# Kernel tuning notes

Measured on AMD Instinct MI355X. Metric: run time of the kernel, lower is better.

Reference implementation:

```python
import jax, jax.numpy as jnp
import numpy as np

HEADS = 16
DIM_HEAD = 64
DIM = 1024
INNER = HEADS * DIM_HEAD


def setup_inputs() -> dict:
    key = jax.random.key(0)
    k1, k2, k3, k4 = jax.random.split(key, 4)
    x = jax.random.normal(k1, (4, 2048, DIM), dtype=jnp.float32)
    W_qkv = jax.random.normal(k2, (DIM, 3 * INNER), dtype=jnp.float32) * (DIM ** -0.5)
    W_out = jax.random.normal(k3, (INNER, DIM), dtype=jnp.float32) * (INNER ** -0.5)
    b_out = jax.random.normal(k4, (DIM,), dtype=jnp.float32) * 0.01
    temperature = jnp.asarray(np.log(DIM_HEAD ** -0.5), dtype=jnp.float32)
    return {"x": x, "W_qkv": W_qkv, "W_out": W_out, "b_out": b_out,
            "temperature": temperature}


def reference(x, W_qkv, W_out, b_out, temperature):
    b, n, _ = x.shape
    qkv = jnp.einsum('bnd,de->bne', x, W_qkv)  # [b, n, 3*inner]
    q, k, v = jnp.split(qkv, 3, axis=-1)
    def split_heads(t):
        return t.reshape(b, n, HEADS, DIM_HEAD).transpose(0, 2, 1, 3)  # b h n d
    q, k, v = split_heads(q), split_heads(k), split_heads(v)
    scale = jnp.exp(temperature)
    dots = jnp.einsum('bhid,bhjd->bhij', q, k) * scale  # [b, h, n, n]
    mask_value = -jnp.finfo(dots.dtype).max
    eye = jnp.eye(n, dtype=bool)
    dots = jnp.where(eye, mask_value, dots)
    attn = jax.nn.softmax(dots, axis=-1)
    out = jnp.einsum('bhij,bhjd->bhid', attn, v)  # [b, h, n, d]
    out = out.transpose(0, 2, 1, 3).reshape(b, n, INNER)
    return jnp.einsum('bni,id->bnd', out, W_out) + b_out
```

## Files before the change

kernel.cpp:

```cpp
#include <hip/hip_runtime.h>


using u16 = unsigned short;
typedef short short8 __attribute__((ext_vector_type(8)));
typedef float floatx4 __attribute__((ext_vector_type(4)));
typedef float floatx16 __attribute__((ext_vector_type(16)));
typedef unsigned int uint2v __attribute__((ext_vector_type(2)));

#define B_ 4
#define N_ 2048
#define H_ 16
#define DH_ 64
#define D_ 1024
#define INNER_ 1024
#define M_ (B_ * N_)

__device__ __forceinline__ float bf2f(u16 h) {
    union { unsigned u; float f; } c; c.u = ((unsigned)h) << 16; return c.f;
}
__device__ __forceinline__ u16 f2bf(float f) {
    union { float f; unsigned u; } c; c.f = f;
    unsigned u = c.u + 0x7fffu + ((c.u >> 16) & 1u);
    return (u16)(u >> 16);
}
__device__ __forceinline__ unsigned cvtpk_bf16(float lo, float hi) {
    unsigned r;
    asm("v_cvt_pk_bf16_f32 %0, %1, %2" : "=v"(r) : "v"(lo), "v"(hi));
    return r;
}
__device__ __forceinline__ float fast_exp2(float x) {
#if defined(__has_builtin) && __has_builtin(__builtin_amdgcn_exp2f)
    return __builtin_amdgcn_exp2f(x);
#else
    return __expf(x * 0.69314718056f);
#endif
}
__device__ __forceinline__ void gl2lds16(const u16* g, u16* l) {
    __builtin_amdgcn_global_load_lds(
        (const __attribute__((address_space(1))) void*)g,
        (__attribute__((address_space(3))) void*)l, 16, 0, 0);
}

__global__ void detect_dtype(const u16* __restrict__ x, int* __restrict__ flag) {
    __shared__ int cnt;
    if (threadIdx.x == 0) cnt = 0;
    __syncthreads();
    int c = 0;
    for (int i = threadIdx.x; i < 4096; i += 256) {
        int e = (x[i] >> 7) & 0xFF;
        if (e >= 107 && e <= 147) c++;
    }
    atomicAdd(&cnt, c);
    __syncthreads();
    if (threadIdx.x == 0) flag[0] = (cnt >= 3584) ? 1 : 0;
}

__global__ __launch_bounds__(256) void convert_x(
    const void* __restrict__ in, u16* __restrict__ out, int n,
    const int* __restrict__ flag) {
    int f = flag[0];
    int i0 = (blockIdx.x * 256 + threadIdx.x) * 8;
    if (f) {
        const u16* p = (const u16*)in;
        for (int i = 0; i < 8; i++) out[i0 + i] = p[i0 + i];
    } else {
        const float* p = (const float*)in;
        for (int i = 0; i < 8; i++) out[i0 + i] = f2bf(p[i0 + i]);
    }
}

__global__ void prep_misc(const void* __restrict__ bias_in,
                          const void* __restrict__ temp_in,
                          float* __restrict__ bias_f, float* __restrict__ temp_f,
                          const int* __restrict__ flag) {
    int f = flag[0];
    for (int i = threadIdx.x; i < 1024; i += 256)
        bias_f[i] = f ? bf2f(((const u16*)bias_in)[i]) : ((const float*)bias_in)[i];
    if (threadIdx.x == 0)
        temp_f[0] = f ? bf2f(((const u16*)temp_in)[0]) : ((const float*)temp_in)[0];
}

__global__ __launch_bounds__(256) void transpose_cvt(
    const void* __restrict__ in, u16* __restrict__ out, int R, int C,
    const int* __restrict__ flag) {
    __shared__ u16 t[32][33];
    int f = flag[0];
    int tx = threadIdx.x & 31, ty = threadIdx.x >> 5;
    int c0 = blockIdx.x * 32, r0 = blockIdx.y * 32;
    for (int i = 0; i < 4; i++) {
        long idx = (long)(r0 + ty + i * 8) * C + c0 + tx;
        t[ty + i * 8][tx] = f ? ((const u16*)in)[idx] : f2bf(((const float*)in)[idx]);
    }
    __syncthreads();
    for (int i = 0; i < 4; i++)
        out[(long)(c0 + ty + i * 8) * R + r0 + tx] = t[tx][ty + i * 8];
}

__global__ __launch_bounds__(256) void transpose_v(
    const u16* __restrict__ in, u16* __restrict__ out) {
    __shared__ u16 t[32][33];
    const int bh = blockIdx.z;
    const u16* src = in + (long)bh * N_ * DH_;
    u16* dst = out + (long)bh * DH_ * N_;
    int tx = threadIdx.x & 31, ty = threadIdx.x >> 5;
    int r0 = blockIdx.y * 32;
    int c0 = blockIdx.x * 32;
    for (int i = 0; i < 4; i++)
        t[ty + i * 8][tx] = src[(long)(r0 + ty + i * 8) * DH_ + c0 + tx];
    __syncthreads();
    for (int i = 0; i < 4; i++)
        dst[(long)(c0 + ty + i * 8) * N_ + r0 + tx] = t[tx][ty + i * 8];
}

template <int MODE>
__global__ __launch_bounds__(256) void gemm_bt(
    const u16* __restrict__ A, const u16* __restrict__ Bt,
    int M, int N, int K,
    u16* __restrict__ out0, u16* __restrict__ out1, u16* __restrict__ out2,
    void* __restrict__ outv, const float* __restrict__ bias,
    const int* __restrict__ flag, const float* __restrict__ temp_f) {
    __shared__ __align__(16) u16 lA[128 * 32];
    __shared__ __align__(16) u16 lB[128 * 32];
    const int tid = threadIdx.x;
    const int lane = tid & 63;
    const int w = tid >> 6;
    const int wr = w >> 1, wc = w & 1;
    const int qd = lane >> 4, qm = lane & 15;
    const long m0 = (long)blockIdx.x * 128;
    const long n0 = (long)blockIdx.y * 128;

    floatx4 acc[4][4];
    for (int i = 0; i < 4; i++)
        for (int j = 0; j < 4; j++) acc[i][j] = (floatx4){0.f, 0.f, 0.f, 0.f};

    const int arow = lane >> 2;
    const int acol = ((lane & 3) ^ ((lane >> 3) & 3)) * 8;
    const int swz = (qm >> 1) & 3;

    for (int k0 = 0; k0 < K; k0 += 32) {
        for (int i = 0; i < 2; i++) {
            int c = w + i * 4;
            gl2lds16(A + (m0 + c * 16 + arow) * K + k0 + acol, lA + c * 512);
            gl2lds16(Bt + (n0 + c * 16 + arow) * K + k0 + acol, lB + c * 512);
        }
        __syncthreads();
        short8 af[4], bfr[4];
        for (int mt = 0; mt < 4; mt++)
            af[mt] = *(const short8*)&lA[(wr * 64 + mt * 16 + qm) * 32 + (qd ^ swz) * 8];
        for (int nt = 0; nt < 4; nt++)
            bfr[nt] = *(const short8*)&lB[(wc * 64 + nt * 16 + qm) * 32 + (qd ^ swz) * 8];
        for (int mt = 0; mt < 4; mt++)
            for (int nt = 0; nt < 4; nt++)
                acc[mt][nt] = __builtin_amdgcn_mfma_f32_16x16x32_bf16(
                    af[mt], bfr[nt], acc[mt][nt], 0, 0, 0);
        __syncthreads();
    }

    if (MODE == 0) {
        const float qscale = __expf(temp_f[0]) * 1.44269504089f;
        __shared__ __align__(16) u16 lC[64 * 132];
        for (int half = 0; half < 2; half++) {
            __syncthreads();
            if (wr == half) {
                for (int nt = 0; nt < 4; nt++) {
                    long ng = n0 + wc * 64 + nt * 16 + qm;
                    float sc = ((ng >> 10) == 0) ? qscale : 1.0f;
                    for (int mt = 0; mt < 4; mt++)
                        for (int r = 0; r < 4; r++)
                            lC[(mt * 16 + qd * 4 + r) * 132 + wc * 64 + nt * 16 + qm] =
                                f2bf(acc[mt][nt][r] * sc);
                }
            }
            __syncthreads();
            for (int i = 0; i < 4; i++) {
                int row = (tid >> 4) + i * 16;
                int c = (tid & 15) * 8;
                long m = m0 + half * 64 + row;
                long ngc = n0 + c;
                int part = (int)(ngc >> 10);
                int rem = (int)(ngc & 1023);
                int hh = rem >> 6, dh = rem & 63;
                long bb = m >> 11, n = m & 2047;
                long idx = ((bb * H_ + hh) * N_ + n) * DH_ + dh;
                short8 vv = *(const short8*)&lC[row * 132 + c];
                u16* dst = (part == 0) ? out0 : (part == 1) ? out1 : out2;
                *(short8*)&dst[idx] = vv;
            }
        }
    } else {
        const int f = flag[0];
        __shared__ __align__(16) float lCf[64 * 132];
        for (int half = 0; half < 2; half++) {
            __syncthreads();
            if (wr == half) {
                for (int nt = 0; nt < 4; nt++) {
                    long ng = n0 + wc * 64 + nt * 16 + qm;
                    float bv = bias[ng];
                    for (int mt = 0; mt < 4; mt++)
                        for (int r = 0; r < 4; r++)
                            lCf[(mt * 16 + qd * 4 + r) * 132 + wc * 64 + nt * 16 + qm] =
                                acc[mt][nt][r] + bv;
                }
            }
            __syncthreads();
            if (f) {
                for (int i = 0; i < 4; i++) {
                    int row = (tid >> 4) + i * 16;
                    int c = (tid & 15) * 8;
                    long m = m0 + half * 64 + row;
                    u16 tmp[8];
                    for (int j = 0; j < 8; j++) tmp[j] = f2bf(lCf[row * 132 + c + j]);
                    *(short8*)&((u16*)outv)[m * N + n0 + c] = *(const short8*)tmp;
                }
            } else {
                for (int i = 0; i < 8; i++) {
                    int row = (tid >> 5) + i * 8;
                    int c = (tid & 31) * 4;
                    long m = m0 + half * 64 + row;
                    floatx4 vv = *(const floatx4*)&lCf[row * 132 + c];
                    *(floatx4*)&((float*)outv)[m * N + n0 + c] = vv;
                }
            }
        }
    }
}

__global__ __launch_bounds__(256) void attn_kernel(
    const u16* __restrict__ q_ws, const u16* __restrict__ k_ws,
    const u16* __restrict__ vt_ws, u16* __restrict__ out) {
    __shared__ __align__(16) u16 lbuf[2 * 2 * 64 * 64];
    const int tid = threadIdx.x, lane = tid & 63, w = tid >> 6;
    const int ln = lane & 31, h = lane >> 5;

    int linear = blockIdx.y * 8 + blockIdx.x;
    int bh = (linear & 7) * 8 + ((linear >> 6) & 7);
    int q0 = ((linear >> 3) & 7) * 256;
    const int b = bh >> 4, hd = bh & 15;

    const u16* Q = q_ws + (long)bh * N_ * DH_;
    const u16* Kp = k_ws + (long)bh * N_ * DH_;
    const u16* Vt = vt_ws + (long)bh * DH_ * N_;

    const int qbase = q0 + w * 64;

    short8 qa[2][4];
#pragma unroll
    for (int g = 0; g < 2; g++)
#pragma unroll
        for (int c = 0; c < 4; c++)
            qa[g][c] = *(const short8*)
                &Q[(long)(qbase + g * 32 + ln) * DH_ + c * 16 + h * 8];

    floatx16 accO[2][2];
#pragma unroll
    for (int i = 0; i < 16; i++) {
        accO[0][0][i] = 0.f; accO[0][1][i] = 0.f;
        accO[1][0][i] = 0.f; accO[1][1][i] = 0.f;
    }
    float lacc[2] = {0.f, 0.f};

    const int srow = lane >> 3;
    const int scol = ((lane & 7) ^ srow) * 8;
    const int rsw = (ln & 7);

    {
        u16* nK = lbuf;
        u16* nV = lbuf + 4096;
        for (int i = 0; i < 2; i++) {
            int c = w + i * 4;
            gl2lds16(Kp + (long)(c * 8 + srow) * DH_ + scol, nK + c * 512);
            gl2lds16(Vt + (long)(c * 8 + srow) * N_ + scol, nV + c * 512);
        }
    }
    __syncthreads();

    for (int t = 0; t < 32; t++) {
        const int k0 = t * 64;
        const u16* lK = lbuf + (t & 1) * 8192;
        const u16* lV = lK + 4096;
        if (t < 31) {
            u16* nK = lbuf + ((t + 1) & 1) * 8192;
            u16* nV = nK + 4096;
            for (int i = 0; i < 2; i++) {
                int c = w + i * 4;
                gl2lds16(Kp + (long)(k0 + 64 + c * 8 + srow) * DH_ + scol,
                         nK + c * 512);
                gl2lds16(Vt + (long)(c * 8 + srow) * N_ + k0 + 64 + scol,
                         nV + c * 512);
            }
        }

#pragma unroll
        for (int kt = 0; kt < 2; kt++) {
            floatx16 accS[2];
#pragma unroll
            for (int i = 0; i < 16; i++) { accS[0][i] = 0.f; accS[1][i] = 0.f; }
#pragma unroll
            for (int c = 0; c < 4; c++) {
                short8 kf = *(const short8*)
                    &lK[(kt * 32 + ln) * 64 + ((c * 2 + h) ^ rsw) * 8];
                accS[0] = __builtin_amdgcn_mfma_f32_32x32x16_bf16(
                    kf, qa[0][c], accS[0], 0, 0, 0);
                accS[1] = __builtin_amdgcn_mfma_f32_32x32x16_bf16(
                    kf, qa[1][c], accS[1], 0, 0, 0);
            }
#pragma unroll
            for (int g = 0; g < 2; g++) {
#pragma unroll
                for (int r = 0; r < 16; r++)
                    accS[g][r] = fast_exp2(accS[g][r]);
                if ((qbase + g * 32) == (k0 + kt * 32)) {
#pragma unroll
                    for (int r = 0; r < 16; r++) {
                        int kk = (r & 3) + 8 * (r >> 2) + 4 * h;
                        if (kk == ln) accS[g][r] = 0.f;
                    }
                }
                float rs = (((accS[g][0] + accS[g][1]) + (accS[g][2] + accS[g][3]))
                          + ((accS[g][4] + accS[g][5]) + (accS[g][6] + accS[g][7])))
                         + (((accS[g][8] + accS[g][9]) + (accS[g][10] + accS[g][11]))
                          + ((accS[g][12] + accS[g][13]) + (accS[g][14] + accS[g][15])));
                lacc[g] += rs;
            }
#pragma unroll
            for (int ch = 0; ch < 2; ch++) {
                const int rb = ch * 8;
                short8 pfv[2];
#pragma unroll
                for (int g = 0; g < 2; g++) {
                    unsigned d01 = cvtpk_bf16(accS[g][rb + 0], accS[g][rb + 1]);
                    unsigned d23 = cvtpk_bf16(accS[g][rb + 2], accS[g][rb + 3]);
                    unsigned d45 = cvtpk_bf16(accS[g][rb + 4], accS[g][rb + 5]);
                    unsigned d67 = cvtpk_bf16(accS[g][rb + 6], accS[g][rb + 7]);
                    uint2v s1 = __builtin_amdgcn_permlane32_swap(d01, d45, false, false);
                    uint2v s2 = __builtin_amdgcn_permlane32_swap(d23, d67, false, false);
                    union { unsigned u[4]; short8 v; } pf;
                    pf.u[0] = s1[0]; pf.u[1] = s2[0]; pf.u[2] = s1[1]; pf.u[3] = s2[1];
                    pfv[g] = pf.v;
                }
                const int cc = kt * 2 + ch;
#pragma unroll
                for (int dt = 0; dt < 2; dt++) {
                    short8 vf = *(const short8*)
                        &lV[(dt * 32 + ln) * 64 + ((cc * 2 + h) ^ rsw) * 8];
                    accO[0][dt] = __builtin_amdgcn_mfma_f32_32x32x16_bf16(
                        vf, pfv[0], accO[0][dt], 0, 0, 0);
                    accO[1][dt] = __builtin_amdgcn_mfma_f32_32x32x16_bf16(
                        vf, pfv[1], accO[1][dt], 0, 0, 0);
                }
            }
        }
        __syncthreads();
    }

#pragma unroll
    for (int g = 0; g < 2; g++) {
        float s = lacc[g];
        s += __shfl_xor(s, 32, 64);
        const float inv = 1.f / s;
        u16* stg = (u16*)((char*)lbuf + w * 8192 + g * 4096);
#pragma unroll
        for (int dt = 0; dt < 2; dt++)
#pragma unroll
            for (int q2 = 0; q2 < 4; q2++) {
                union { unsigned u[2]; unsigned long long ull; } ee;
                ee.u[0] = cvtpk_bf16(accO[g][dt][q2 * 4 + 0] * inv,
                                     accO[g][dt][q2 * 4 + 1] * inv);
                ee.u[1] = cvtpk_bf16(accO[g][dt][q2 * 4 + 2] * inv,
                                     accO[g][dt][q2 * 4 + 3] * inv);
                int G = dt * 4 + q2;
                *(unsigned long long*)
                    &stg[ln * 64 + ((G ^ rsw) * 8) + h * 4] = ee.ull;
            }
    }
    __syncthreads();
#pragma unroll
    for (int p = 0; p < 8; p++) {
        int R = p * 32 + (tid >> 3);
        int G = tid & 7;
        const u16* src = (const u16*)((char*)lbuf + (R >> 6) * 8192
                          + ((R >> 5) & 1) * 4096
                          + (R & 31) * 128 + ((G ^ (R & 7)) * 16));
        short8 vv = *(const short8*)src;
        *(short8*)&out[((long)(b * N_ + q0 + R)) * INNER_ + hd * DH_ + G * 8] = vv;
    }
}

extern "C" void kernel_launch(void* const* d_in, const int* in_sizes, int n_in,
                              void* d_out, int out_size, void* d_ws, size_t ws_size,
                              hipStream_t stream) {
    const void* x    = d_in[0];
    const void* Wqkv = d_in[1];
    const void* Wout = d_in[2];
    const void* bout = d_in[3];
    const void* temp = d_in[4];

    char* base = (char*)d_ws;
    int*   flag    = (int*)base;
    float* temp_f  = (float*)(base + 16);
    float* bias_f  = (float*)(base + 32);
    u16* xb      = (u16*)(base + 8192);
    u16* Wqkv_t  = xb + (long)M_ * D_;
    u16* Wout_t  = Wqkv_t + 3072 * 1024;
    u16* q_ws    = Wout_t + 1024 * 1024;
    u16* k_ws    = q_ws + (long)B_ * H_ * N_ * DH_;
    u16* vt_ws   = k_ws + (long)B_ * H_ * N_ * DH_;
    u16* attn_out = vt_ws + (long)B_ * H_ * N_ * DH_;
    u16* v_nat   = attn_out;

    dim3 blk(256);
    detect_dtype<<<1, blk, 0, stream>>>((const u16*)x, flag);
    convert_x<<<dim3(M_ * D_ / (256 * 8)), blk, 0, stream>>>(x, xb, M_ * D_, flag);
    prep_misc<<<1, blk, 0, stream>>>(bout, temp, bias_f, temp_f, flag);
    transpose_cvt<<<dim3(3 * INNER_ / 32, D_ / 32), blk, 0, stream>>>(
        Wqkv, Wqkv_t, D_, 3 * INNER_, flag);
    transpose_cvt<<<dim3(D_ / 32, INNER_ / 32), blk, 0, stream>>>(
        Wout, Wout_t, INNER_, D_, flag);
    gemm_bt<0><<<dim3(M_ / 128, 3 * INNER_ / 128), blk, 0, stream>>>(
        xb, Wqkv_t, M_, 3 * INNER_, D_, q_ws, k_ws, v_nat, nullptr, nullptr,
        flag, temp_f);
    transpose_v<<<dim3(DH_ / 32, N_ / 32, B_ * H_), blk, 0, stream>>>(
        v_nat, vt_ws);
    attn_kernel<<<dim3(N_ / 256, B_ * H_), blk, 0, stream>>>(
        q_ws, k_ws, vt_ws, attn_out);
    gemm_bt<1><<<dim3(M_ / 128, D_ / 128), blk, 0, stream>>>(
        attn_out, Wout_t, M_, D_, INNER_, nullptr, nullptr, nullptr, d_out,
        bias_f, flag, temp_f);
}
```

Before: 302.7 us.

## Shrink attention blocks to two waves with 128 queries and refine LDS swizzle

Attention blocks now have 128 threads (2 waves) covering 128 query rows instead of 256 threads covering 256, doubling the grid to 1024 blocks. Each wave now loads twice as many K/V chunks into LDS, and the swizzle adds an extra XOR bit on row bit 3 to reduce bank conflicts. The grid remap and the output staging addresses were updated to match. The aim is better CU occupancy and load balance across the 256 CUs, at the cost of more K/V global traffic per query, since each K/V tile is loaded once per 128 queries instead of once per 256.

Measured after the change: 305.4 us. Within noise of the previous version (+0.9%).

```diff
diff --git a/kernel.cpp b/kernel.cpp
--- a/kernel.cpp
+++ b/kernel.cpp
@@ -225,16 +225,16 @@
     }
 }
 
-__global__ __launch_bounds__(256) void attn_kernel(
+__global__ __launch_bounds__(128) void attn_kernel(
     const u16* __restrict__ q_ws, const u16* __restrict__ k_ws,
     const u16* __restrict__ vt_ws, u16* __restrict__ out) {
     __shared__ __align__(16) u16 lbuf[2 * 2 * 64 * 64];
     const int tid = threadIdx.x, lane = tid & 63, w = tid >> 6;
     const int ln = lane & 31, h = lane >> 5;
 
-    int linear = blockIdx.y * 8 + blockIdx.x;
-    int bh = (linear & 7) * 8 + ((linear >> 6) & 7);
-    int q0 = ((linear >> 3) & 7) * 256;
+    int linear = blockIdx.y * 16 + blockIdx.x;
+    int bh = (linear & 7) * 8 + (linear >> 7);
+    int q0 = ((linear >> 3) & 15) * 128;
     const int b = bh >> 4, hd = bh & 15;
 
     const u16* Q = q_ws + (long)bh * N_ * DH_;
@@ -260,17 +260,15 @@
     float lacc[2] = {0.f, 0.f};
 
     const int srow = lane >> 3;
-    const int scol = ((lane & 7) ^ srow) * 8;
-    const int rsw = (ln & 7);
-
-    {
-        u16* nK = lbuf;
-        u16* nV = lbuf + 4096;
-        for (int i = 0; i < 2; i++) {
-            int c = w + i * 4;
-            gl2lds16(Kp + (long)(c * 8 + srow) * DH_ + scol, nK + c * 512);
-            gl2lds16(Vt + (long)(c * 8 + srow) * N_ + scol, nV + c * 512);
-        }
+    const int l7 = lane & 7;
+    const int rsw = (ln & 7) ^ ((ln & 8) >> 1);
+
+#pragma unroll
+    for (int i = 0; i < 4; i++) {
+        int c = w * 4 + i;
+        int sc = (l7 ^ srow ^ ((c & 1) << 2)) * 8;
+        gl2lds16(Kp + (long)(c * 8 + srow) * DH_ + sc, lbuf + c * 512);
+        gl2lds16(Vt + (long)(c * 8 + srow) * N_ + sc, lbuf + 4096 + c * 512);
     }
     __syncthreads();
 
@@ -281,11 +279,13 @@
         if (t < 31) {
             u16* nK = lbuf + ((t + 1) & 1) * 8192;
             u16* nV = nK + 4096;
-            for (int i = 0; i < 2; i++) {
-                int c = w + i * 4;
-                gl2lds16(Kp + (long)(k0 + 64 + c * 8 + srow) * DH_ + scol,
+#pragma unroll
+            for (int i = 0; i < 4; i++) {
+                int c = w * 4 + i;
+                int sc = (l7 ^ srow ^ ((c & 1) << 2)) * 8;
+                gl2lds16(Kp + (long)(k0 + 64 + c * 8 + srow) * DH_ + sc,
                          nK + c * 512);
-                gl2lds16(Vt + (long)(c * 8 + srow) * N_ + k0 + 64 + scol,
+                gl2lds16(Vt + (long)(c * 8 + srow) * N_ + k0 + 64 + sc,
                          nV + c * 512);
             }
         }
@@ -358,7 +358,7 @@
         float s = lacc[g];
         s += __shfl_xor(s, 32, 64);
         const float inv = 1.f / s;
-        u16* stg = (u16*)((char*)lbuf + w * 8192 + g * 4096);
+        u16* stg = lbuf + w * 4096 + g * 2048;
 #pragma unroll
         for (int dt = 0; dt < 2; dt++)
 #pragma unroll
@@ -376,11 +376,11 @@
     __syncthreads();
 #pragma unroll
     for (int p = 0; p < 8; p++) {
-        int R = p * 32 + (tid >> 3);
+        int R = p * 16 + (tid >> 3);
         int G = tid & 7;
-        const u16* src = (const u16*)((char*)lbuf + (R >> 6) * 8192
-                          + ((R >> 5) & 1) * 4096
-                          + (R & 31) * 128 + ((G ^ (R & 7)) * 16));
+        int gran = G ^ (R & 7) ^ ((R & 8) >> 1);
+        const u16* src = lbuf + (R >> 6) * 4096 + ((R >> 5) & 1) * 2048
+                         + (R & 31) * 64 + gran * 8;
         short8 vv = *(const short8*)src;
         *(short8*)&out[((long)(b * N_ + q0 + R)) * INNER_ + hd * DH_ + G * 8] = vv;
     }
@@ -421,7 +421,7 @@
         flag, temp_f);
     transpose_v<<<dim3(DH_ / 32, N_ / 32, B_ * H_), blk, 0, stream>>>(
         v_nat, vt_ws);
-    attn_kernel<<<dim3(N_ / 256, B_ * H_), blk, 0, stream>>>(
+    attn_kernel<<<dim3(N_ / 128, B_ * H_), dim3(128), 0, stream>>>(
         q_ws, k_ws, vt_ws, attn_out);
     gemm_bt<1><<<dim3(M_ / 128, D_ / 128), blk, 0, stream>>>(
         attn_out, Wout_t, M_, D_, INNER_, nullptr, nullptr, nullptr, d_out,
```

## Split attention over two key halves with fp32 partials and merge kernel

Applied to the files above, without the earlier changes.

Adds a split-K attention path where each block processes half of the keys, writing unnormalized fp32 partial outputs and row sums, followed by a merge kernel that sums, normalizes and converts to bf16. This doubles the attention grid to improve CU occupancy and load balance. It costs extra global traffic for fp32 partials and another launch, and is only taken when workspace is large enough.

Result: slower. 316.8 us (+4.6%).

```diff
diff --git a/kernel.cpp b/kernel.cpp
--- a/kernel.cpp
+++ b/kernel.cpp
@@ -225,7 +225,7 @@
     }
 }
 
-__global__ __launch_bounds__(256) void attn_kernel(
+__global__ __launch_bounds__(256) void attn_full(
     const u16* __restrict__ q_ws, const u16* __restrict__ k_ws,
     const u16* __restrict__ vt_ws, u16* __restrict__ out) {
     __shared__ __align__(16) u16 lbuf[2 * 2 * 64 * 64];
@@ -386,6 +386,199 @@
     }
 }
 
+__global__ __launch_bounds__(256) void attn_split(
+    const u16* __restrict__ q_ws, const u16* __restrict__ k_ws,
+    const u16* __restrict__ vt_ws, float* __restrict__ part,
+    float* __restrict__ lsum) {
+    __shared__ __align__(16) u16 lbuf[2 * 2 * 64 * 64];
+    const int tid = threadIdx.x, lane = tid & 63, w = tid >> 6;
+    const int ln = lane & 31, h = lane >> 5;
+
+    int linear = blockIdx.y * 16 + blockIdx.x;
+    int bh = (linear & 7) * 8 + ((linear >> 7) & 7);
+    int q0 = ((linear >> 3) & 7) * 256;
+    int kh = (linear >> 6) & 1;
+    const int kbase = kh * 1024;
+
+    const u16* Q = q_ws + (long)bh * N_ * DH_;
+    const u16* Kp = k_ws + (long)bh * N_ * DH_;
+    const u16* Vt = vt_ws + (long)bh * DH_ * N_;
+
+    const int qbase = q0 + w * 64;
+
+    short8 qa[2][4];
+#pragma unroll
+    for (int g = 0; g < 2; g++)
+#pragma unroll
+        for (int c = 0; c < 4; c++)
+            qa[g][c] = *(const short8*)
+                &Q[(long)(qbase + g * 32 + ln) * DH_ + c * 16 + h * 8];
+
+    floatx16 accO[2][2];
+#pragma unroll
+    for (int i = 0; i < 16; i++) {
+        accO[0][0][i] = 0.f; accO[0][1][i] = 0.f;
+        accO[1][0][i] = 0.f; accO[1][1][i] = 0.f;
+    }
+    float lacc[2] = {0.f, 0.f};
+
+    const int srow = lane >> 3;
+    const int scol = ((lane & 7) ^ srow) * 8;
+    const int rsw = (ln & 7);
+
+    {
+        u16* nK = lbuf;
+        u16* nV = lbuf + 4096;
+        for (int i = 0; i < 2; i++) {
+            int c = w + i * 4;
+            gl2lds16(Kp + (long)(kbase + c * 8 + srow) * DH_ + scol, nK + c * 512);
+            gl2lds16(Vt + (long)(c * 8 + srow) * N_ + kbase + scol, nV + c * 512);
+        }
+    }
+    __syncthreads();
+
+    for (int t = 0; t < 16; t++) {
+        const int k0 = kbase + t * 64;
+        const u16* lK = lbuf + (t & 1) * 8192;
+        const u16* lV = lK + 4096;
+        if (t < 15) {
+            u16* nK = lbuf + ((t + 1) & 1) * 8192;
+            u16* nV = nK + 4096;
+            for (int i = 0; i < 2; i++) {
+                int c = w + i * 4;
+                gl2lds16(Kp + (long)(k0 + 64 + c * 8 + srow) * DH_ + scol,
+                         nK + c * 512);
+                gl2lds16(Vt + (long)(c * 8 + srow) * N_ + k0 + 64 + scol,
+                         nV + c * 512);
+            }
+        }
+
+#pragma unroll
+        for (int kt = 0; kt < 2; kt++) {
+            floatx16 accS[2];
+#pragma unroll
+            for (int i = 0; i < 16; i++) { accS[0][i] = 0.f; accS[1][i] = 0.f; }
+#pragma unroll
+            for (int c = 0; c < 4; c++) {
+                short8 kf = *(const short8*)
+                    &lK[(kt * 32 + ln) * 64 + ((c * 2 + h) ^ rsw) * 8];
+                accS[0] = __builtin_amdgcn_mfma_f32_32x32x16_bf16(
+                    kf, qa[0][c], accS[0], 0, 0, 0);
+                accS[1] = __builtin_amdgcn_mfma_f32_32x32x16_bf16(
+                    kf, qa[1][c], accS[1], 0, 0, 0);
+            }
+#pragma unroll
+            for (int g = 0; g < 2; g++) {
+#pragma unroll
+                for (int r = 0; r < 16; r++)
+                    accS[g][r] = fast_exp2(accS[g][r]);
+                if ((qbase + g * 32) == (k0 + kt * 32)) {
+#pragma unroll
+                    for (int r = 0; r < 16; r++) {
+                        int kk = (r & 3) + 8 * (r >> 2) + 4 * h;
+                        if (kk == ln) accS[g][r] = 0.f;
+                    }
+                }
+                float rs = (((accS[g][0] + accS[g][1]) + (accS[g][2] + accS[g][3]))
+                          + ((accS[g][4] + accS[g][5]) + (accS[g][6] + accS[g][7])))
+                         + (((accS[g][8] + accS[g][9]) + (accS[g][10] + accS[g][11]))
+                          + ((accS[g][12] + accS[g][13]) + (accS[g][14] + accS[g][15])));
+                lacc[g] += rs;
+            }
+#pragma unroll
+            for (int ch = 0; ch < 2; ch++) {
+                const int rb = ch * 8;
+                short8 pfv[2];
+#pragma unroll
+                for (int g = 0; g < 2; g++) {
+                    unsigned d01 = cvtpk_bf16(accS[g][rb + 0], accS[g][rb + 1]);
+                    unsigned d23 = cvtpk_bf16(accS[g][rb + 2], accS[g][rb + 3]);
+                    unsigned d45 = cvtpk_bf16(accS[g][rb + 4], accS[g][rb + 5]);
+                    unsigned d67 = cvtpk_bf16(accS[g][rb + 6], accS[g][rb + 7]);
+                    uint2v s1 = __builtin_amdgcn_permlane32_swap(d01, d45, false, false);
+                    uint2v s2 = __builtin_amdgcn_permlane32_swap(d23, d67, false, false);
+                    union { unsigned u[4]; short8 v; } pf;
+                    pf.u[0] = s1[0]; pf.u[1] = s2[0]; pf.u[2] = s1[1]; pf.u[3] = s2[1];
+                    pfv[g] = pf.v;
+                }
+                const int cc = kt * 2 + ch;
+#pragma unroll
+                for (int dt = 0; dt < 2; dt++) {
+                    short8 vf = *(const short8*)
+                        &lV[(dt * 32 + ln) * 64 + ((cc * 2 + h) ^ rsw) * 8];
+                    accO[0][dt] = __builtin_amdgcn_mfma_f32_32x32x16_bf16(
+                        vf, pfv[0], accO[0][dt], 0, 0, 0);
+                    accO[1][dt] = __builtin_amdgcn_mfma_f32_32x32x16_bf16(
+                        vf, pfv[1], accO[1][dt], 0, 0, 0);
+                }
+            }
+        }
+        __syncthreads();
+    }
+
+    float* pbase = part + ((long)kh * 64 + bh) * N_ * DH_;
+#pragma unroll
+    for (int g = 0; g < 2; g++) {
+        __syncthreads();
+        float* stg = (float*)lbuf + w * 2048;
+#pragma unroll
+        for (int dt = 0; dt < 2; dt++)
+#pragma unroll
+            for (int q2 = 0; q2 < 4; q2++) {
+                int c4 = dt * 8 + 2 * q2 + h;
+                int g4 = c4 ^ (ln & 15);
+                floatx4 v4;
+                v4[0] = accO[g][dt][q2 * 4 + 0];
+                v4[1] = accO[g][dt][q2 * 4 + 1];
+                v4[2] = accO[g][dt][q2 * 4 + 2];
+                v4[3] = accO[g][dt][q2 * 4 + 3];
+                *(floatx4*)&stg[ln * 64 + g4 * 4] = v4;
+            }
+        __syncthreads();
+#pragma unroll
+        for (int p = 0; p < 8; p++) {
+            int i = p * 256 + tid;
+            int wv = i >> 9;
+            int row = (i >> 4) & 31;
+            int c4 = i & 15;
+            const float* src = (const float*)lbuf + wv * 2048 + row * 64
+                               + (c4 ^ (row & 15)) * 4;
+            floatx4 v4 = *(const floatx4*)src;
+            long qrow = q0 + wv * 64 + g * 32 + row;
+            *(floatx4*)&pbase[qrow * DH_ + c4 * 4] = v4;
+        }
+    }
+#pragma unroll
+    for (int g = 0; g < 2; g++) {
+        float s = lacc[g] + __shfl_xor(lacc[g], 32, 64);
+        if (h == 0)
+            lsum[((long)kh * 64 + bh) * N_ + q0 + w * 64 + g * 32 + ln] = s;
+    }
+}
+
+__global__ __launch_bounds__(256) void merge_attn(
+    const float* __restrict__ part, const float* __restrict__ lsum,
+    u16* __restrict__ out) {
+    long i0 = ((long)blockIdx.x * 256 + threadIdx.x) * 8;
+    long row = i0 >> 10;
+    int col = (int)(i0 & 1023);
+    int h = col >> 6, dh = col & 63;
+    long bh = (row >> 11) * 16 + h;
+    long q = row & 2047;
+    const float* p0 = part + (bh * N_ + q) * DH_ + dh;
+    const float* p1 = part + ((64 + bh) * N_ + q) * DH_ + dh;
+    float l = lsum[bh * N_ + q] + lsum[(64 + bh) * N_ + q];
+    float inv = 1.f / l;
+    floatx4 a0 = *(const floatx4*)p0, a1 = *(const floatx4*)(p0 + 4);
+    floatx4 b0 = *(const floatx4*)p1, b1 = *(const floatx4*)(p1 + 4);
+    union { unsigned u[4]; short8 v; } oo;
+    oo.u[0] = cvtpk_bf16((a0[0] + b0[0]) * inv, (a0[1] + b0[1]) * inv);
+    oo.u[1] = cvtpk_bf16((a0[2] + b0[2]) * inv, (a0[3] + b0[3]) * inv);
+    oo.u[2] = cvtpk_bf16((a1[0] + b1[0]) * inv, (a1[1] + b1[1]) * inv);
+    oo.u[3] = cvtpk_bf16((a1[2] + b1[2]) * inv, (a1[3] + b1[3]) * inv);
+    *(short8*)&out[i0] = oo.v;
+}
+
 extern "C" void kernel_launch(void* const* d_in, const int* in_sizes, int n_in,
                               void* d_out, int out_size, void* d_ws, size_t ws_size,
                               hipStream_t stream) {
@@ -407,6 +600,9 @@
     u16* vt_ws   = k_ws + (long)B_ * H_ * N_ * DH_;
     u16* attn_out = vt_ws + (long)B_ * H_ * N_ * DH_;
     u16* v_nat   = attn_out;
+    float* part  = (float*)(attn_out + (long)M_ * INNER_);
+    float* lsum  = part + 2L * 64 * N_ * DH_;
+    const int use_split = (ws_size >= (size_t)160440320ULL) ? 1 : 0;
 
     dim3 blk(256);
     detect_dtype<<<1, blk, 0, stream>>>((const u16*)x, flag);
@@ -421,8 +617,15 @@
         flag, temp_f);
     transpose_v<<<dim3(DH_ / 32, N_ / 32, B_ * H_), blk, 0, stream>>>(
         v_nat, vt_ws);
-    attn_kernel<<<dim3(N_ / 256, B_ * H_), blk, 0, stream>>>(
-        q_ws, k_ws, vt_ws, attn_out);
+    if (use_split) {
+        attn_split<<<dim3(16, 64), blk, 0, stream>>>(
+            q_ws, k_ws, vt_ws, part, lsum);
+        merge_attn<<<dim3(M_ * INNER_ / (256 * 8)), blk, 0, stream>>>(
+            part, lsum, attn_out);
+    } else {
+        attn_full<<<dim3(8, 64), blk, 0, stream>>>(
+            q_ws, k_ws, vt_ws, attn_out);
+    }
     gemm_bt<1><<<dim3(M_ / 128, D_ / 128), blk, 0, stream>>>(
         attn_out, Wout_t, M_, D_, INNER_, nullptr, nullptr, nullptr, d_out,
         bias_f, flag, temp_f);
```
